# Kernel optimization log

Hardware: AMD Instinct MI355X
Metric: run time of the kernel (lower is better)

Reference implementation:

```python
import jax, jax.numpy as jnp
import numpy as np


def _grid_sample_3d(vol, pts):
    """Trilinear grid_sample, align_corners=True, padding_mode='border'.
    vol: [C, D, H, W]; pts: [N, 3] with (x, y, z) in normalized [-1, 1] coords
    (x indexes W, y indexes H, z indexes D, matching torch.grid_sample).
    Returns [N, C]."""
    C, D, H, W = vol.shape
    def to_idx(c, size):
        c = (c + 1.0) * 0.5 * (size - 1)
        return jnp.clip(c, 0.0, size - 1.0)  # border padding
    ix = to_idx(pts[:, 0], W)
    iy = to_idx(pts[:, 1], H)
    iz = to_idx(pts[:, 2], D)
    x0 = jnp.floor(ix); y0 = jnp.floor(iy); z0 = jnp.floor(iz)
    wx = ix - x0;       wy = iy - y0;       wz = iz - z0
    x0i = x0.astype(jnp.int32); x1i = jnp.minimum(x0i + 1, W - 1)
    y0i = y0.astype(jnp.int32); y1i = jnp.minimum(y0i + 1, H - 1)
    z0i = z0.astype(jnp.int32); z1i = jnp.minimum(z0i + 1, D - 1)
    g = lambda zi, yi, xi: vol[:, zi, yi, xi]  # [C, N]
    out = (g(z0i, y0i, x0i) * (1 - wz) * (1 - wy) * (1 - wx)
         + g(z0i, y0i, x1i) * (1 - wz) * (1 - wy) * wx
         + g(z0i, y1i, x0i) * (1 - wz) * wy * (1 - wx)
         + g(z0i, y1i, x1i) * (1 - wz) * wy * wx
         + g(z1i, y0i, x0i) * wz * (1 - wy) * (1 - wx)
         + g(z1i, y0i, x1i) * wz * (1 - wy) * wx
         + g(z1i, y1i, x0i) * wz * wy * (1 - wx)
         + g(z1i, y1i, x1i) * wz * wy * wx)
    return out.T  # [N, C]


def _skinning(x, w, tfs):
    """x: [B,N,3], w: [B,N,J], tfs: [B,J,4,4] -> (xd [B,N,3], w_tf [B,N,4,4])."""
    x_h = jnp.concatenate([x, jnp.ones_like(x[..., :1])], axis=-1)  # [B,N,4]
    w_tf = jnp.einsum('bpn,bnij->bpij', w, tfs)                      # [B,N,4,4]
    xh = jnp.einsum('bpij,bpj->bpi', w_tf, x_h)                      # [B,N,4]
    return xh[..., :3], w_tf


def setup_inputs() -> dict:
    key = jax.random.key(0)
    ks = jax.random.split(key, 12)
    B, N, J = 4, 250000, 55
    return {
        'xc': jax.random.normal(ks[0], (B, N, 3), jnp.float32),
        'shape_offset': jax.random.normal(ks[1], (B, N, 3), jnp.float32),
        'pose_offset': jax.random.normal(ks[2], (B, N, 3), jnp.float32),
        'tfs': jax.random.normal(ks[3], (B, J, 4, 4), jnp.float32),
        'tfs_inv': jax.random.normal(ks[4], (1, J, 4, 4), jnp.float32),
        'poseoff_ori': jax.random.normal(ks[5], (1, N, 3), jnp.float32),
        'lbsw': jax.random.uniform(ks[6], (1, N, J), jnp.float32),
        'mask': jax.random.randint(ks[7], (1, N), 0, 2).astype(bool),
        'lbs_voxel': jax.random.uniform(ks[8], (1, J, 16, 64, 64), jnp.float32),
        'offset_kernel': jnp.zeros((1, 1, 3), jnp.float32),
        'scale_kernel': jax.random.uniform(ks[9], (1, 1, 3), jnp.float32),
    }


def reference(xc, shape_offset, pose_offset, tfs, tfs_inv, poseoff_ori,
              lbsw, mask, lbs_voxel, offset_kernel, scale_kernel):
    B = xc.shape[0]
    # query_weights: normalize then trilinear grid sample of shared voxel
    xn = (xc + offset_kernel) * scale_kernel  # [B,N,3]
    vol = lbs_voxel[0]                        # [J,16,64,64], shared across batch
    w = jax.vmap(lambda p: _grid_sample_3d(vol, p))(xn)  # [B,N,J]
    # w[:, mask[0]] = lbsw[mask]
    w = jnp.where(mask[0][None, :, None], lbsw, w)
    # first blend: canonical with tfs_inv (inverse=False path)
    xc_cano, w_tf_inv = _skinning(xc, w, jnp.broadcast_to(tfs_inv, (B,) + tfs_inv.shape[1:]))
    xc_cano_ori = xc_cano - poseoff_ori
    xc_shape = xc_cano_ori + shape_offset + pose_offset
    # second blend: posed with tfs
    xd, w_tf = _skinning(xc_shape, w, tfs)
    w_tf_all = w_tf @ w_tf_inv  # [B,N,4,4] batched 4x4 matmul
    return xd, w_tf_all
```

## Files before the change

### kernel.cpp

```cpp
#include <hip/hip_runtime.h>
#include <hip/hip_fp16.h>


#define JNT 55
#define VD  16
#define VH  64
#define VW  64
#define NVOX (VD * VH * VW)

__global__ __launch_bounds__(256, 2) void build_tab_k(
    const float* __restrict__ vol, const float* __restrict__ tfs,
    const float* __restrict__ tfs_inv, __half* __restrict__ tab)
{
    int v = blockIdx.x * 256 + threadIdx.x;
    int b = blockIdx.y;
    if (v >= NVOX) return;
    float w[JNT];
#pragma unroll
    for (int j = 0; j < JNT; ++j) w[j] = vol[j * NVOX + v];

    float Mi[16], Mv[16];
#pragma unroll
    for (int i = 0; i < 16; ++i) { Mi[i] = 0.f; Mv[i] = 0.f; }
    const float* tb = tfs + (size_t)b * JNT * 16;
#pragma unroll
    for (int j = 0; j < JNT; ++j) {
        float wj = w[j];
#pragma unroll
        for (int i = 0; i < 16; ++i) Mi[i] = fmaf(wj, tfs_inv[j * 16 + i], Mi[i]);
#pragma unroll
        for (int i = 0; i < 16; ++i) Mv[i] = fmaf(wj, tb[j * 16 + i], Mv[i]);
    }
    float h[16];
#pragma unroll
    for (int i = 0; i < 8; ++i)
        h[i] = __builtin_bit_cast(float, __floats2half2_rn(Mi[2*i], Mi[2*i+1]));
#pragma unroll
    for (int i = 0; i < 8; ++i)
        h[8+i] = __builtin_bit_cast(float, __floats2half2_rn(Mv[2*i], Mv[2*i+1]));

    float4* d4 = (float4*)(tab + ((size_t)b * NVOX + v) * 32);
    d4[0] = make_float4(h[0],  h[1],  h[2],  h[3]);
    d4[1] = make_float4(h[4],  h[5],  h[6],  h[7]);
    d4[2] = make_float4(h[8],  h[9],  h[10], h[11]);
    d4[3] = make_float4(h[12], h[13], h[14], h[15]);
}

__device__ __forceinline__ void acc8(float cw, float4 r, float* a)
{
    float rr[4] = {r.x, r.y, r.z, r.w};
#pragma unroll
    for (int kk = 0; kk < 4; ++kk) {
        __half2 h = __builtin_bit_cast(__half2, rr[kk]);
        float2 f = __half22float2(h);
        a[2*kk]     = fmaf(cw, f.x, a[2*kk]);
        a[2*kk + 1] = fmaf(cw, f.y, a[2*kk + 1]);
    }
}

__device__ __forceinline__ void epilogue(
    int b, int n, int N, float x, float y, float z,
    const float* A, const float* Ai,
    const float* __restrict__ shoff, const float* __restrict__ pooff,
    const float* __restrict__ poori,
    float* __restrict__ out_xd, float* __restrict__ out_w)
{
    size_t pid = (size_t)b * N + n;
    size_t p3  = pid * 3;
    size_t n3  = (size_t)n * 3;
    float c0 = Ai[0]*x + Ai[1]*y + Ai[2]*z  + Ai[3];
    float c1 = Ai[4]*x + Ai[5]*y + Ai[6]*z  + Ai[7];
    float c2 = Ai[8]*x + Ai[9]*y + Ai[10]*z + Ai[11];
    float sx = c0 - poori[n3 + 0] + shoff[p3 + 0] + pooff[p3 + 0];
    float sy = c1 - poori[n3 + 1] + shoff[p3 + 1] + pooff[p3 + 1];
    float sz = c2 - poori[n3 + 2] + shoff[p3 + 2] + pooff[p3 + 2];
    out_xd[p3 + 0] = A[0]*sx + A[1]*sy + A[2]*sz  + A[3];
    out_xd[p3 + 1] = A[4]*sx + A[5]*sy + A[6]*sz  + A[7];
    out_xd[p3 + 2] = A[8]*sx + A[9]*sy + A[10]*sz + A[11];

    float4* ow = (float4*)(out_w + pid * 16);
#pragma unroll
    for (int i = 0; i < 4; ++i) {
        float a0 = A[i*4+0], a1 = A[i*4+1], a2 = A[i*4+2], a3 = A[i*4+3];
        float4 r;
        r.x = a0*Ai[0] + a1*Ai[4] + a2*Ai[8]  + a3*Ai[12];
        r.y = a0*Ai[1] + a1*Ai[5] + a2*Ai[9]  + a3*Ai[13];
        r.z = a0*Ai[2] + a1*Ai[6] + a2*Ai[10] + a3*Ai[14];
        r.w = a0*Ai[3] + a1*Ai[7] + a2*Ai[11] + a3*Ai[15];
        ow[i] = r;
    }
}

template <int B>
__global__ __launch_bounds__(256, 4) void main_k(
    const float* __restrict__ xc,
    const float* __restrict__ shoff,
    const float* __restrict__ pooff,
    const float* __restrict__ tfs,
    const float* __restrict__ tfs_inv,
    const float* __restrict__ poori,
    const float* __restrict__ lbsw,
    const int*   __restrict__ mask,
    const __half* __restrict__ tab,
    const float* __restrict__ offk,
    const float* __restrict__ sck,
    float* __restrict__ out_xd,
    float* __restrict__ out_w,
    int N)
{
    __shared__ float sTi[JNT * 16];
    __shared__ float sT[JNT * B * 16];
    for (int t = threadIdx.x; t < JNT * 16; t += 256) sTi[t] = tfs_inv[t];
    for (int t = threadIdx.x; t < JNT * B * 16; t += 256) {
        int j = t >> 6, r = t & 63, b = r >> 4, i = r & 15;
        sT[t] = tfs[((size_t)b * JNT + j) * 16 + i];
    }
    __syncthreads();

    int tx = threadIdx.x;
    int team = tx >> 2, k = tx & 3;
    int lane = tx & 63, qb = lane & ~3;
    int n = blockIdx.x * 64 + team;
    if (n >= N) return;

    size_t p3 = ((size_t)k * N + n) * 3;
    float x = xc[p3], y = xc[p3 + 1], z = xc[p3 + 2];
    float o0 = offk[0], o1 = offk[1], o2 = offk[2];
    float s0 = sck[0],  s1 = sck[1],  s2 = sck[2];

    float Af[16], Aif[16];
    bool m = (mask[n] != 0);

    if (m) {
        float wl[14];
        const float* row = lbsw + (size_t)n * JNT;
#pragma unroll
        for (int i = 0; i < 14; ++i) {
            int j = 4 * i + k;
            wl[i] = (j < JNT) ? row[j] : 0.f;
        }
        float AiR[4] = {0.f, 0.f, 0.f, 0.f};
#pragma unroll
        for (int i = 0; i < 16; ++i) Af[i] = 0.f;

#pragma unroll
        for (int i = 0; i < 14; ++i) {
#pragma unroll
            for (int k2 = 0; k2 < 4; ++k2) {
                int j = 4 * i + k2;
                if (j >= JNT) continue;
                float wj = __shfl(wl[i], qb + k2);
                float4 ti = *(const float4*)(sTi + j * 16 + 4 * k);
                AiR[0] = fmaf(wj, ti.x, AiR[0]);
                AiR[1] = fmaf(wj, ti.y, AiR[1]);
                AiR[2] = fmaf(wj, ti.z, AiR[2]);
                AiR[3] = fmaf(wj, ti.w, AiR[3]);
                const float* tb = sT + (j * B + k) * 16;
#pragma unroll
                for (int q = 0; q < 4; ++q) {
                    float4 r = *(const float4*)(tb + 4 * q);
                    Af[4*q+0] = fmaf(wj, r.x, Af[4*q+0]);
                    Af[4*q+1] = fmaf(wj, r.y, Af[4*q+1]);
                    Af[4*q+2] = fmaf(wj, r.z, Af[4*q+2]);
                    Af[4*q+3] = fmaf(wj, r.w, Af[4*q+3]);
                }
            }
        }
#pragma unroll
        for (int r = 0; r < 4; ++r)
#pragma unroll
            for (int i = 0; i < 4; ++i)
                Aif[r * 4 + i] = __shfl(AiR[i], qb + r);
    } else {
#pragma unroll
        for (int b = 0; b < B; ++b) {
            float xb = __shfl(x, qb + b);
            float yb = __shfl(y, qb + b);
            float zb = __shfl(z, qb + b);
            float px = (xb + o0) * s0;
            float py = (yb + o1) * s1;
            float pz = (zb + o2) * s2;
            float ix = fminf(fmaxf((px + 1.f) * 0.5f * (VW - 1), 0.f), (float)(VW - 1));
            float iy = fminf(fmaxf((py + 1.f) * 0.5f * (VH - 1), 0.f), (float)(VH - 1));
            float iz = fminf(fmaxf((pz + 1.f) * 0.5f * (VD - 1), 0.f), (float)(VD - 1));
            float fx = floorf(ix), fy = floorf(iy), fz = floorf(iz);
            float wx = ix - fx,    wy = iy - fy,    wz = iz - fz;
            int x0 = (int)fx, y0 = (int)fy, z0 = (int)fz;
            int x1 = min(x0 + 1, VW - 1);
            int y1 = min(y0 + 1, VH - 1);
            int z1 = min(z0 + 1, VD - 1);
            float cwx[2] = {1.f - wx, wx};
            float cwy[2] = {1.f - wy, wy};
            float cwz[2] = {1.f - wz, wz};
            int   xs[2] = {x0, x1}, ys[2] = {y0, y1}, zs[2] = {z0, z1};

            float acc[8];
#pragma unroll
            for (int i = 0; i < 8; ++i) acc[i] = 0.f;
            const __half* tbb = tab + (size_t)b * NVOX * 32;
#pragma unroll
            for (int c = 0; c < 8; ++c) {
                int cz = c >> 2, cy = (c >> 1) & 1, cx = c & 1;
                int vox = (zs[cz] * VH + ys[cy]) * VW + xs[cx];
                float cw = cwz[cz] * cwy[cy] * cwx[cx];
                float4 r4 = ((const float4*)(tbb + (size_t)vox * 32))[k];
                acc8(cw, r4, acc);
            }
#pragma unroll
            for (int i = 0; i < 8; ++i) {
#pragma unroll
                for (int j2 = 0; j2 < 4; ++j2) {
                    float v = __shfl(acc[i], qb + j2);
                    int dst = 8 * j2 + i;
                    if (k == b) {
                        if (dst < 16) Aif[dst] = v;
                        else          Af[dst - 16] = v;
                    }
                }
            }
        }
    }

    epilogue(k, n, N, x, y, z, Af, Aif, shoff, pooff, poori, out_xd, out_w);
}

__global__ __launch_bounds__(256) void fb_k(
    const float* __restrict__ xc, const float* __restrict__ shoff,
    const float* __restrict__ pooff, const float* __restrict__ tfs,
    const float* __restrict__ tfs_inv, const float* __restrict__ poori,
    const float* __restrict__ lbsw, const int* __restrict__ mask,
    const float* __restrict__ vol, const float* __restrict__ offk,
    const float* __restrict__ sck, float* __restrict__ out_xd,
    float* __restrict__ out_w, int N)
{
    int n = blockIdx.x * 256 + threadIdx.x;
    int b = blockIdx.y;
    if (n >= N) return;
    size_t p3 = ((size_t)b * N + n) * 3;
    float x = xc[p3], y = xc[p3 + 1], z = xc[p3 + 2];
    float A[16], Ai[16];
#pragma unroll
    for (int i = 0; i < 16; ++i) { A[i] = 0.f; Ai[i] = 0.f; }
    const float* tb = tfs + (size_t)b * JNT * 16;

    if (mask[n] != 0) {
        const float* lp = lbsw + (size_t)n * JNT;
        for (int j = 0; j < JNT; ++j) {
            float wj = lp[j];
#pragma unroll
            for (int i = 0; i < 16; ++i) Ai[i] = fmaf(wj, tfs_inv[j*16+i], Ai[i]);
#pragma unroll
            for (int i = 0; i < 16; ++i) A[i]  = fmaf(wj, tb[j*16+i],      A[i]);
        }
    } else {
        float px = (x + offk[0]) * sck[0];
        float py = (y + offk[1]) * sck[1];
        float pz = (z + offk[2]) * sck[2];
        float ix = fminf(fmaxf((px + 1.f) * 0.5f * (VW - 1), 0.f), (float)(VW - 1));
        float iy = fminf(fmaxf((py + 1.f) * 0.5f * (VH - 1), 0.f), (float)(VH - 1));
        float iz = fminf(fmaxf((pz + 1.f) * 0.5f * (VD - 1), 0.f), (float)(VD - 1));
        float fx = floorf(ix), fy = floorf(iy), fz = floorf(iz);
        float wx = ix - fx, wy = iy - fy, wz = iz - fz;
        int x0 = (int)fx, y0 = (int)fy, z0 = (int)fz;
        int x1 = min(x0 + 1, VW - 1);
        int y1 = min(y0 + 1, VH - 1);
        int z1 = min(z0 + 1, VD - 1);
        float w00 = (1.f - wz) * (1.f - wy), w01 = (1.f - wz) * wy;
        float w10 = wz * (1.f - wy),         w11 = wz * wy;
        int o00 = (z0 * VH + y0) * VW, o01 = (z0 * VH + y1) * VW;
        int o10 = (z1 * VH + y0) * VW, o11 = (z1 * VH + y1) * VW;
        for (int j = 0; j < JNT; ++j) {
            const float* vp = vol + (size_t)j * NVOX;
            float v000 = vp[o00 + x0], v001 = vp[o00 + x1];
            float v010 = vp[o01 + x0], v011 = vp[o01 + x1];
            float v100 = vp[o10 + x0], v101 = vp[o10 + x1];
            float v110 = vp[o11 + x0], v111 = vp[o11 + x1];
            float c0 = w00 * v000 + w01 * v010 + w10 * v100 + w11 * v110;
            float c1 = w00 * v001 + w01 * v011 + w10 * v101 + w11 * v111;
            float wj = c0 + wx * (c1 - c0);
#pragma unroll
            for (int i = 0; i < 16; ++i) Ai[i] = fmaf(wj, tfs_inv[j*16+i], Ai[i]);
#pragma unroll
            for (int i = 0; i < 16; ++i) A[i]  = fmaf(wj, tb[j*16+i],      A[i]);
        }
    }
    epilogue(b, n, N, x, y, z, A, Ai, shoff, pooff, poori, out_xd, out_w);
}

extern "C" void kernel_launch(void* const* d_in, const int* in_sizes, int n_in,
                              void* d_out, int out_size, void* d_ws, size_t ws_size,
                              hipStream_t stream)
{
    const float* xc    = (const float*)d_in[0];
    const float* shoff = (const float*)d_in[1];
    const float* pooff = (const float*)d_in[2];
    const float* tfs   = (const float*)d_in[3];
    const float* tfsi  = (const float*)d_in[4];
    const float* poori = (const float*)d_in[5];
    const float* lbsw  = (const float*)d_in[6];
    const int*   mask  = (const int*)d_in[7];
    const float* vol   = (const float*)d_in[8];
    const float* offk  = (const float*)d_in[9];
    const float* sck   = (const float*)d_in[10];

    int N = in_sizes[5] / 3;
    int B = in_sizes[0] / (3 * N);
    float* out_xd = (float*)d_out;
    float* out_w  = (float*)d_out + (size_t)B * N * 3;

    size_t tab_bytes = (size_t)B * NVOX * 32 * sizeof(__half);
    __half* tab = (__half*)d_ws;

    if (B == 4 && ws_size >= tab_bytes) {
        build_tab_k<<<dim3((NVOX + 255) / 256, 4), dim3(256), 0, stream>>>(
            vol, tfs, tfsi, tab);
        main_k<4><<<dim3((N + 63) / 64), dim3(256), 0, stream>>>(
            xc, shoff, pooff, tfs, tfsi, poori, lbsw, mask, tab,
            offk, sck, out_xd, out_w, N);
    } else {
        fb_k<<<dim3((N + 255) / 256, B), dim3(256), 0, stream>>>(
            xc, shoff, pooff, tfs, tfsi, poori, lbsw, mask, vol, offk, sck,
            out_xd, out_w, N);
    }
}
```

Before: 285.7 us.

## Compact masked points per block and transpose trilinear accumulators via butterfly shuffles

Each block now ballots the mask over its 64 points and permutes them so masked points sit in the leading teams. Whole wavefronts then take one branch instead of diverging between the lbsw path and the voxel path. The unmasked path also replaces the 32-shuffle-per-batch broadcast with per-batch accumulators and a two-stage xor butterfly transpose, which cuts shuffle count. The cost is extra shared memory and a sync-dependent permutation, plus more registers for the 32-float result array.

```diff
diff --git a/kernel.cpp b/kernel.cpp
--- a/kernel.cpp
+++ b/kernel.cpp
@@ -110,26 +110,38 @@
 {
     __shared__ float sTi[JNT * 16];
     __shared__ float sT[JNT * B * 16];
-    for (int t = threadIdx.x; t < JNT * 16; t += 256) sTi[t] = tfs_inv[t];
-    for (int t = threadIdx.x; t < JNT * B * 16; t += 256) {
+    __shared__ unsigned char sPerm[64];
+    __shared__ int sNm;
+
+    int tx = threadIdx.x;
+    for (int t = tx; t < JNT * 16; t += 256) sTi[t] = tfs_inv[t];
+    for (int t = tx; t < JNT * B * 16; t += 256) {
         int j = t >> 6, r = t & 63, b = r >> 4, i = r & 15;
         sT[t] = tfs[((size_t)b * JNT + j) * 16 + i];
     }
+    if (tx < 64) {
+        int n0 = blockIdx.x * 64 + tx;
+        bool mm = (n0 < N) && (mask[n0] != 0);
+        unsigned long long bal = __ballot(mm);
+        int nm = __popcll(bal);
+        unsigned long long below = bal & ((1ull << tx) - 1ull);
+        int pos = mm ? __popcll(below) : (nm + (tx - __popcll(below)));
+        sPerm[pos] = (unsigned char)tx;
+        if (tx == 0) sNm = nm;
+    }
     __syncthreads();
 
-    int tx = threadIdx.x;
     int team = tx >> 2, k = tx & 3;
     int lane = tx & 63, qb = lane & ~3;
-    int n = blockIdx.x * 64 + team;
+    int slot = sPerm[team];
+    int n = blockIdx.x * 64 + slot;
+    bool m = (team < sNm);
     if (n >= N) return;
 
     size_t p3 = ((size_t)k * N + n) * 3;
     float x = xc[p3], y = xc[p3 + 1], z = xc[p3 + 2];
-    float o0 = offk[0], o1 = offk[1], o2 = offk[2];
-    float s0 = sck[0],  s1 = sck[1],  s2 = sck[2];
-
-    float Af[16], Aif[16];
-    bool m = (mask[n] != 0);
+
+    float res[32];
 
     if (m) {
         float wl[14];
@@ -141,7 +153,7 @@
         }
         float AiR[4] = {0.f, 0.f, 0.f, 0.f};
 #pragma unroll
-        for (int i = 0; i < 16; ++i) Af[i] = 0.f;
+        for (int i = 0; i < 16; ++i) res[16 + i] = 0.f;
 
 #pragma unroll
         for (int i = 0; i < 14; ++i) {
@@ -159,10 +171,10 @@
 #pragma unroll
                 for (int q = 0; q < 4; ++q) {
                     float4 r = *(const float4*)(tb + 4 * q);
-                    Af[4*q+0] = fmaf(wj, r.x, Af[4*q+0]);
-                    Af[4*q+1] = fmaf(wj, r.y, Af[4*q+1]);
-                    Af[4*q+2] = fmaf(wj, r.z, Af[4*q+2]);
-                    Af[4*q+3] = fmaf(wj, r.w, Af[4*q+3]);
+                    res[16 + 4*q + 0] = fmaf(wj, r.x, res[16 + 4*q + 0]);
+                    res[16 + 4*q + 1] = fmaf(wj, r.y, res[16 + 4*q + 1]);
+                    res[16 + 4*q + 2] = fmaf(wj, r.z, res[16 + 4*q + 2]);
+                    res[16 + 4*q + 3] = fmaf(wj, r.w, res[16 + 4*q + 3]);
                 }
             }
         }
@@ -170,8 +182,13 @@
         for (int r = 0; r < 4; ++r)
 #pragma unroll
             for (int i = 0; i < 4; ++i)
-                Aif[r * 4 + i] = __shfl(AiR[i], qb + r);
+                res[r * 4 + i] = __shfl(AiR[i], qb + r);
     } else {
+        float o0 = offk[0], o1 = offk[1], o2 = offk[2];
+        float s0 = sck[0],  s1 = sck[1],  s2 = sck[2];
+#pragma unroll
+        for (int i = 0; i < 32; ++i) res[i] = 0.f;
+
 #pragma unroll
         for (int b = 0; b < B; ++b) {
             float xb = __shfl(x, qb + b);
@@ -194,9 +211,6 @@
             float cwz[2] = {1.f - wz, wz};
             int   xs[2] = {x0, x1}, ys[2] = {y0, y1}, zs[2] = {z0, z1};
 
-            float acc[8];
-#pragma unroll
-            for (int i = 0; i < 8; ++i) acc[i] = 0.f;
             const __half* tbb = tab + (size_t)b * NVOX * 32;
 #pragma unroll
             for (int c = 0; c < 8; ++c) {
@@ -204,24 +218,44 @@
                 int vox = (zs[cz] * VH + ys[cy]) * VW + xs[cx];
                 float cw = cwz[cz] * cwy[cy] * cwx[cx];
                 float4 r4 = ((const float4*)(tbb + (size_t)vox * 32))[k];
-                acc8(cw, r4, acc);
+                acc8(cw, r4, res + b * 8);
             }
-#pragma unroll
-            for (int i = 0; i < 8; ++i) {
-#pragma unroll
-                for (int j2 = 0; j2 < 4; ++j2) {
-                    float v = __shfl(acc[i], qb + j2);
-                    int dst = 8 * j2 + i;
-                    if (k == b) {
-                        if (dst < 16) Aif[dst] = v;
-                        else          Af[dst - 16] = v;
-                    }
+        }
+        {
+            int p1 = lane ^ 1;
+            bool odd = (k & 1) != 0;
+#pragma unroll
+            for (int pb = 0; pb < 4; pb += 2) {
+#pragma unroll
+                for (int i = 0; i < 8; ++i) {
+                    float send = odd ? res[pb*8 + i] : res[(pb+1)*8 + i];
+                    float got  = __shfl(send, p1);
+                    float nb   = odd ? got : res[pb*8 + i];
+                    float nb1  = odd ? res[(pb+1)*8 + i] : got;
+                    res[pb*8 + i]     = nb;
+                    res[(pb+1)*8 + i] = nb1;
                 }
             }
         }
-    }
-
-    epilogue(k, n, N, x, y, z, Af, Aif, shoff, pooff, poori, out_xd, out_w);
+        {
+            int p2 = lane ^ 2;
+            bool hi = (k & 2) != 0;
+#pragma unroll
+            for (int pb = 0; pb < 2; ++pb) {
+#pragma unroll
+                for (int i = 0; i < 8; ++i) {
+                    float send = hi ? res[pb*8 + i] : res[(pb+2)*8 + i];
+                    float got  = __shfl(send, p2);
+                    float nb   = hi ? got : res[pb*8 + i];
+                    float nb2  = hi ? res[(pb+2)*8 + i] : got;
+                    res[pb*8 + i]     = nb;
+                    res[(pb+2)*8 + i] = nb2;
+                }
+            }
+        }
+    }
+
+    epilogue(k, n, N, x, y, z, res + 16, res, shoff, pooff, poori, out_xd, out_w);
 }
 
 __global__ __launch_bounds__(256) void fb_k(
```

After: 293.7 us. 2.8% more time.

## Switch main kernel to one thread per point with mask-compacted warps

Applied to the files above, without the earlier changes.

Replaces the 4-thread team per point (one lane per batch, exchanging data through shuffles) with one thread per (point, batch), using a 2D grid over batches. Inside each block, points are reordered with ballot/popcount so masked and unmasked points sit in separate contiguous warps, which cuts divergence between the lbsw-blend path and the table-lookup path. The masked path now reads transforms from global or constant-cached memory instead of shared staging, and the lookup path loads all four float4 chunks of a voxel entry per thread. In exchange, lbsw rows are re-read once per batch and the permutation breaks coalescing of per-point loads.

```diff
diff --git a/kernel.cpp b/kernel.cpp
--- a/kernel.cpp
+++ b/kernel.cpp
@@ -7,6 +7,8 @@
 #define VH  64
 #define VW  64
 #define NVOX (VD * VH * VW)
+
+typedef float f4u __attribute__((ext_vector_type(4), aligned(4)));
 
 __global__ __launch_bounds__(256, 2) void build_tab_k(
     const float* __restrict__ vol, const float* __restrict__ tfs,
@@ -108,120 +110,100 @@
     float* __restrict__ out_w,
     int N)
 {
-    __shared__ float sTi[JNT * 16];
-    __shared__ float sT[JNT * B * 16];
-    for (int t = threadIdx.x; t < JNT * 16; t += 256) sTi[t] = tfs_inv[t];
-    for (int t = threadIdx.x; t < JNT * B * 16; t += 256) {
-        int j = t >> 6, r = t & 63, b = r >> 4, i = r & 15;
-        sT[t] = tfs[((size_t)b * JNT + j) * 16 + i];
-    }
+    __shared__ unsigned short sPerm[256];
+    __shared__ int sCnt[4];
+
+    int tx = threadIdx.x;
+    int b  = blockIdx.y;
+    int base = blockIdx.x * 256;
+
+    int wv = tx >> 6, ln = tx & 63;
+    int n0 = base + tx;
+    bool mm = (n0 < N) && (mask[n0] != 0);
+    unsigned long long bal = __ballot(mm);
+    int cm = __popcll(bal);
+    if (ln == 0) sCnt[wv] = cm;
     __syncthreads();
-
-    int tx = threadIdx.x;
-    int team = tx >> 2, k = tx & 3;
-    int lane = tx & 63, qb = lane & ~3;
-    int n = blockIdx.x * 64 + team;
+    int c0 = sCnt[0], c1 = sCnt[1], c2 = sCnt[2], c3 = sCnt[3];
+    int totM  = c0 + c1 + c2 + c3;
+    int mBase = (wv > 0 ? c0 : 0) + (wv > 1 ? c1 : 0) + (wv > 2 ? c2 : 0);
+    unsigned long long below = bal & ((1ull << ln) - 1ull);
+    int rm  = __popcll(below);
+    int pos = mm ? (mBase + rm) : (totM + (wv * 64 - mBase) + (ln - rm));
+    sPerm[pos] = (unsigned short)tx;
+    __syncthreads();
+
+    int slot = sPerm[tx];
+    int n = base + slot;
+    bool m = (tx < totM);
     if (n >= N) return;
 
-    size_t p3 = ((size_t)k * N + n) * 3;
+    size_t p3 = ((size_t)b * N + n) * 3;
     float x = xc[p3], y = xc[p3 + 1], z = xc[p3 + 2];
-    float o0 = offk[0], o1 = offk[1], o2 = offk[2];
-    float s0 = sck[0],  s1 = sck[1],  s2 = sck[2];
-
-    float Af[16], Aif[16];
-    bool m = (mask[n] != 0);
+
+    float A[16], Ai[16];
+#pragma unroll
+    for (int i = 0; i < 16; ++i) { A[i] = 0.f; Ai[i] = 0.f; }
 
     if (m) {
-        float wl[14];
+        const float* tb  = tfs + (size_t)b * JNT * 16;
         const float* row = lbsw + (size_t)n * JNT;
 #pragma unroll
-        for (int i = 0; i < 14; ++i) {
-            int j = 4 * i + k;
-            wl[i] = (j < JNT) ? row[j] : 0.f;
-        }
-        float AiR[4] = {0.f, 0.f, 0.f, 0.f};
-#pragma unroll
-        for (int i = 0; i < 16; ++i) Af[i] = 0.f;
-
-#pragma unroll
-        for (int i = 0; i < 14; ++i) {
-#pragma unroll
-            for (int k2 = 0; k2 < 4; ++k2) {
-                int j = 4 * i + k2;
-                if (j >= JNT) continue;
-                float wj = __shfl(wl[i], qb + k2);
-                float4 ti = *(const float4*)(sTi + j * 16 + 4 * k);
-                AiR[0] = fmaf(wj, ti.x, AiR[0]);
-                AiR[1] = fmaf(wj, ti.y, AiR[1]);
-                AiR[2] = fmaf(wj, ti.z, AiR[2]);
-                AiR[3] = fmaf(wj, ti.w, AiR[3]);
-                const float* tb = sT + (j * B + k) * 16;
-#pragma unroll
-                for (int q = 0; q < 4; ++q) {
-                    float4 r = *(const float4*)(tb + 4 * q);
-                    Af[4*q+0] = fmaf(wj, r.x, Af[4*q+0]);
-                    Af[4*q+1] = fmaf(wj, r.y, Af[4*q+1]);
-                    Af[4*q+2] = fmaf(wj, r.z, Af[4*q+2]);
-                    Af[4*q+3] = fmaf(wj, r.w, Af[4*q+3]);
-                }
+        for (int jj = 0; jj < 13; ++jj) {
+            f4u w4 = *(const f4u*)(row + 4 * jj);
+            float wq[4] = {w4.x, w4.y, w4.z, w4.w};
+#pragma unroll
+            for (int q = 0; q < 4; ++q) {
+                int j = 4 * jj + q;
+                float wj = wq[q];
+#pragma unroll
+                for (int i = 0; i < 16; ++i) Ai[i] = fmaf(wj, tfs_inv[j*16+i], Ai[i]);
+#pragma unroll
+                for (int i = 0; i < 16; ++i) A[i]  = fmaf(wj, tb[j*16+i],      A[i]);
             }
         }
 #pragma unroll
-        for (int r = 0; r < 4; ++r)
-#pragma unroll
-            for (int i = 0; i < 4; ++i)
-                Aif[r * 4 + i] = __shfl(AiR[i], qb + r);
+        for (int j = 52; j < JNT; ++j) {
+            float wj = row[j];
+#pragma unroll
+            for (int i = 0; i < 16; ++i) Ai[i] = fmaf(wj, tfs_inv[j*16+i], Ai[i]);
+#pragma unroll
+            for (int i = 0; i < 16; ++i) A[i]  = fmaf(wj, tb[j*16+i],      A[i]);
+        }
     } else {
-#pragma unroll
-        for (int b = 0; b < B; ++b) {
-            float xb = __shfl(x, qb + b);
-            float yb = __shfl(y, qb + b);
-            float zb = __shfl(z, qb + b);
-            float px = (xb + o0) * s0;
-            float py = (yb + o1) * s1;
-            float pz = (zb + o2) * s2;
-            float ix = fminf(fmaxf((px + 1.f) * 0.5f * (VW - 1), 0.f), (float)(VW - 1));
-            float iy = fminf(fmaxf((py + 1.f) * 0.5f * (VH - 1), 0.f), (float)(VH - 1));
-            float iz = fminf(fmaxf((pz + 1.f) * 0.5f * (VD - 1), 0.f), (float)(VD - 1));
-            float fx = floorf(ix), fy = floorf(iy), fz = floorf(iz);
-            float wx = ix - fx,    wy = iy - fy,    wz = iz - fz;
-            int x0 = (int)fx, y0 = (int)fy, z0 = (int)fz;
-            int x1 = min(x0 + 1, VW - 1);
-            int y1 = min(y0 + 1, VH - 1);
-            int z1 = min(z0 + 1, VD - 1);
-            float cwx[2] = {1.f - wx, wx};
-            float cwy[2] = {1.f - wy, wy};
-            float cwz[2] = {1.f - wz, wz};
-            int   xs[2] = {x0, x1}, ys[2] = {y0, y1}, zs[2] = {z0, z1};
-
-            float acc[8];
-#pragma unroll
-            for (int i = 0; i < 8; ++i) acc[i] = 0.f;
-            const __half* tbb = tab + (size_t)b * NVOX * 32;
-#pragma unroll
-            for (int c = 0; c < 8; ++c) {
-                int cz = c >> 2, cy = (c >> 1) & 1, cx = c & 1;
-                int vox = (zs[cz] * VH + ys[cy]) * VW + xs[cx];
-                float cw = cwz[cz] * cwy[cy] * cwx[cx];
-                float4 r4 = ((const float4*)(tbb + (size_t)vox * 32))[k];
-                acc8(cw, r4, acc);
-            }
-#pragma unroll
-            for (int i = 0; i < 8; ++i) {
-#pragma unroll
-                for (int j2 = 0; j2 < 4; ++j2) {
-                    float v = __shfl(acc[i], qb + j2);
-                    int dst = 8 * j2 + i;
-                    if (k == b) {
-                        if (dst < 16) Aif[dst] = v;
-                        else          Af[dst - 16] = v;
-                    }
-                }
-            }
-        }
-    }
-
-    epilogue(k, n, N, x, y, z, Af, Aif, shoff, pooff, poori, out_xd, out_w);
+        float px = (x + offk[0]) * sck[0];
+        float py = (y + offk[1]) * sck[1];
+        float pz = (z + offk[2]) * sck[2];
+        float ix = fminf(fmaxf((px + 1.f) * 0.5f * (VW - 1), 0.f), (float)(VW - 1));
+        float iy = fminf(fmaxf((py + 1.f) * 0.5f * (VH - 1), 0.f), (float)(VH - 1));
+        float iz = fminf(fmaxf((pz + 1.f) * 0.5f * (VD - 1), 0.f), (float)(VD - 1));
+        float fx = floorf(ix), fy = floorf(iy), fz = floorf(iz);
+        float wx = ix - fx,    wy = iy - fy,    wz = iz - fz;
+        int x0 = (int)fx, y0 = (int)fy, z0 = (int)fz;
+        int x1 = min(x0 + 1, VW - 1);
+        int y1 = min(y0 + 1, VH - 1);
+        int z1 = min(z0 + 1, VD - 1);
+        float cwx[2] = {1.f - wx, wx};
+        float cwy[2] = {1.f - wy, wy};
+        float cwz[2] = {1.f - wz, wz};
+        int   xs[2] = {x0, x1}, ys[2] = {y0, y1}, zs[2] = {z0, z1};
+
+        const __half* tbb = tab + (size_t)b * NVOX * 32;
+#pragma unroll
+        for (int c = 0; c < 8; ++c) {
+            int cz = c >> 2, cy = (c >> 1) & 1, cx = c & 1;
+            int vox = (zs[cz] * VH + ys[cy]) * VW + xs[cx];
+            float cw = cwz[cz] * cwy[cy] * cwx[cx];
+            const float4* e = (const float4*)(tbb + (size_t)vox * 32);
+            float4 e0 = e[0], e1 = e[1], e2 = e[2], e3 = e[3];
+            acc8(cw, e0, Ai);
+            acc8(cw, e1, Ai + 8);
+            acc8(cw, e2, A);
+            acc8(cw, e3, A + 8);
+        }
+    }
+
+    epilogue(b, n, N, x, y, z, A, Ai, shoff, pooff, poori, out_xd, out_w);
 }
 
 __global__ __launch_bounds__(256) void fb_k(
@@ -314,7 +296,7 @@
     if (B == 4 && ws_size >= tab_bytes) {
         build_tab_k<<<dim3((NVOX + 255) / 256, 4), dim3(256), 0, stream>>>(
             vol, tfs, tfsi, tab);
-        main_k<4><<<dim3((N + 63) / 64), dim3(256), 0, stream>>>(
+        main_k<4><<<dim3((N + 255) / 256, 4), dim3(256), 0, stream>>>(
             xc, shoff, pooff, tfs, tfsi, poori, lbsw, mask, tab,
             offk, sck, out_xd, out_w, N);
     } else {
```

New measurement: 450.7 us. +57.8%, slower.
